# Optimization experiments

Measured on AMD Instinct MI355X. Metric: run time of the kernel, lower is better.

## Reference

```python
import jax, jax.numpy as jnp
import numpy as np

EPS = 1e-8
MARGIN = 0.2
LAMBDA_SM_LSE = 6.0   # i2t attention smooth (opt.lambda_softmax_lse)
LAMBDA_SM_AVG = 9.0   # t2i attention smooth (opt.lambda_softmax_avg)
LAMBDA_LSE = 6.0      # LogSumExp aggregation temperature
NEG = -1e9


def _l2norm(x, axis):
    return x / (jnp.sqrt(jnp.sum(x * x, axis=axis, keepdims=True)) + EPS)


def _cos(a, b):
    # cosine over last axis, torch-style: w12 / clamp(|a||b|, eps)
    w12 = jnp.sum(a * b, axis=-1)
    w1 = jnp.sqrt(jnp.sum(a * a, axis=-1))
    w2 = jnp.sqrt(jnp.sum(b * b, axis=-1))
    return w12 / jnp.maximum(w1 * w2, EPS)


def _forward(im, s, s_l):
    B, R, D = im.shape
    W = s.shape[1]
    wmask = jnp.arange(W)[None, :] < s_l[:, None]          # (Bc, W) valid words
    s = s * wmask[:, :, None]                              # emulate ragged slice s[j,:len_j]

    # ---------------- i2t: query=image regions, context=caption words ----------
    # attn[i,j,w,r] = <s[j,w], im[i,r]>
    A = jnp.einsum('jwd,ird->ijwr', s, im)
    A = jax.nn.leaky_relu(A, 0.1)
    A = _l2norm(A, axis=3)                                 # clipped_l2norm over regions
    logits = jnp.swapaxes(A, 2, 3) * LAMBDA_SM_LSE         # (i,j,r,w), softmax over words
    logits = jnp.where(wmask[None, :, None, :], logits, NEG)
    attn_i2t = jax.nn.softmax(logits, axis=-1)
    wc_t = jnp.einsum('ijrw,jwd->ijrd', attn_i2t, s)       # weighted caption ctx per region
    sim1 = _cos(im[:, None, :, :], wc_t)                   # (i,j,r)
    score1 = jnp.log(jnp.sum(jnp.exp(LAMBDA_LSE * sim1), axis=2)) / LAMBDA_LSE  # (i,j)
    attn_t_full = jnp.mean(wc_t, axis=2)                   # (i,j,d)
    idx = jnp.arange(B)
    attn_t = attn_t_full[idx, idx]                         # (B,d) diagonal

    # ---------------- t2i: query=caption words, context=image regions ----------
    # attn[i,j,r,w] = <im[i,r], s[j,w]>
    Bm = jnp.einsum('ird,jwd->ijrw', im, s)
    Bm = jax.nn.leaky_relu(Bm, 0.1)
    Bm = Bm * wmask[None, :, None, :]                      # padded-word cols excluded from norm
    Bm = _l2norm(Bm, axis=3)                               # clipped_l2norm over words
    logits2 = jnp.swapaxes(Bm, 2, 3) * LAMBDA_SM_AVG       # (i,j,w,r), softmax over regions
    attn_t2i = jax.nn.softmax(logits2, axis=-1)
    wc_i = jnp.einsum('ijwr,ird->ijwd', attn_t2i, im)      # weighted image ctx per word
    sim2 = _cos(s[None, :, :, :], wc_i)                    # (i,j,w)
    e2 = jnp.where(wmask[None, :, :], jnp.exp(LAMBDA_LSE * sim2), 0.0)
    score2 = jnp.log(jnp.sum(e2, axis=2)) / LAMBDA_LSE     # masked LogSumExp over words
    wsum = jnp.sum(wc_i * wmask[None, :, :, None], axis=2)
    attn_i_full = wsum / s_l[None, :, None].astype(wc_i.dtype)  # masked mean over words
    attn_i = attn_i_full[idx, idx]                         # (B,d)

    # ---------------- hinge loss over (B,B) score matrix -----------------------
    scores = 0.5 * (score1 + score2)
    diag = jnp.diagonal(scores)
    cost_s = jnp.maximum(MARGIN + scores - diag[:, None], 0.0)
    cost_im = jnp.maximum(MARGIN + scores - diag[None, :], 0.0)
    eye = jnp.eye(B, dtype=bool)
    cost_s = jnp.where(eye, 0.0, cost_s)
    cost_im = jnp.where(eye, 0.0, cost_im)
    # max_violation=True
    loss = jnp.sum(jnp.max(cost_s, axis=1)) + jnp.sum(jnp.max(cost_im, axis=0))
    return loss, attn_t, attn_i


def setup_inputs() -> dict:
    key = jax.random.key(0)
    k1, k2, k3 = jax.random.split(key, 3)
    B, R, W, D = 64, 36, 40, 1024
    im = jax.random.normal(k1, (B, R, D), dtype=jnp.float32)
    s = jax.random.normal(k2, (B, W, D), dtype=jnp.float32)
    s_l = jax.random.randint(k3, (B,), 10, W + 1)
    return {"im": im, "s": s, "s_l": s_l}


def reference(im, s, s_l):
    return _forward(im, s, s_l)
```

## Files before the change

### kernel.cpp

```cpp
#include <hip/hip_runtime.h>
#include <math.h>

#define Bn 64
#define Rr 36
#define Ww 40
#define Dd 1024
#define GM 2304
#define GN 2560
#define NCONV 4864
#define PAD 72
#define SBP 64
#define TSZ 1440
#define EPSf 1e-8f

typedef unsigned short u16;
typedef __attribute__((ext_vector_type(8))) short bf16x8;
typedef __attribute__((ext_vector_type(4))) float f32x4;

struct alignas(8) U16x4 { u16 x, y, z, w; };

__device__ inline u16 f2bf(float x) {
    unsigned int u = __float_as_uint(x);
    u += 0x7FFFu + ((u >> 16) & 1u);
    return (u16)(u >> 16);
}
__device__ inline float bf2f(u16 h) {
    return __uint_as_float(((unsigned int)h) << 16);
}

__device__ __forceinline__ void gl_lds16(const u16* g, u16* l) {
    __builtin_amdgcn_global_load_lds(
        (const __attribute__((address_space(1))) void*)g,
        (__attribute__((address_space(3))) void*)l, 16, 0, 0);
}

__global__ __launch_bounds__(256) void prep_kernel(const float* __restrict__ im,
                                                   const float* __restrict__ s,
                                                   const int* __restrict__ s_l,
                                                   u16* __restrict__ Ab,
                                                   u16* __restrict__ Bb,
                                                   u16* __restrict__ SSb,
                                                   u16* __restrict__ IIb,
                                                   float* __restrict__ SSd,
                                                   float* __restrict__ IId) {
    __shared__ float red[3][64][37];
    int b = blockIdx.x, t = threadIdx.x;
    if (b < NCONV) {
        const int nA4 = GM * Dd / 4;
        int idx = b * 256 + t;
        if (idx < nA4) {
            float4 v = *(const float4*)(im + (size_t)idx * 4);
            U16x4 o = {f2bf(v.x), f2bf(v.y), f2bf(v.z), f2bf(v.w)};
            *(U16x4*)(Ab + (size_t)idx * 4) = o;
        } else {
            int i2 = idx - nA4;
            int f = i2 * 4;
            int row = f >> 10;
            int j = row / Ww, w = row - j * Ww;
            U16x4 o = {0, 0, 0, 0};
            if (w < s_l[j]) {
                float4 v = *(const float4*)(s + (size_t)f);
                o.x = f2bf(v.x); o.y = f2bf(v.y); o.z = f2bf(v.z); o.w = f2bf(v.w);
            }
            *(U16x4*)(Bb + (size_t)i2 * 4) = o;
        }
        return;
    }
    int gb = b - NCONV;
    bool isS = gb < Bn;
    int idx = isS ? gb : gb - Bn;
    int n = isS ? Ww : Rr;
    const float* basef = isS ? (s + (size_t)idx * Ww * Dd) : (im + (size_t)idx * Rr * Dd);
    u16* outb = isS ? (SSb + (size_t)idx * 48 * SBP) : (IIb + (size_t)idx * 48 * SBP);
    float* outd = isS ? (SSd + (size_t)idx * Ww) : (IId + (size_t)idx * Rr);
    int lane = t & 63, wid = t >> 6;
    int frow = lane & 15, fk = (lane >> 4) * 8;

    f32x4 acc[3][3];
    for (int m = 0; m < 3; ++m)
        for (int p = 0; p < 3; ++p) acc[m][p] = (f32x4){0.f, 0.f, 0.f, 0.f};

    for (int ks = 0; ks < 8; ++ks) {
        int k0 = wid * 256 + ks * 32 + fk;
        bf16x8 f[3];
        for (int m = 0; m < 3; ++m) {
            int rr = m * 16 + frow;
            if (rr >= n) rr = n - 1;
            const float* p = basef + (size_t)rr * Dd + k0;
            float4 v0 = *(const float4*)p;
            float4 v1 = *(const float4*)(p + 4);
            bf16x8 fv;
            fv[0] = (short)f2bf(v0.x); fv[1] = (short)f2bf(v0.y);
            fv[2] = (short)f2bf(v0.z); fv[3] = (short)f2bf(v0.w);
            fv[4] = (short)f2bf(v1.x); fv[5] = (short)f2bf(v1.y);
            fv[6] = (short)f2bf(v1.z); fv[7] = (short)f2bf(v1.w);
            f[m] = fv;
        }
        for (int m = 0; m < 3; ++m)
            for (int p = 0; p < 3; ++p)
                acc[m][p] = __builtin_amdgcn_mfma_f32_16x16x32_bf16(f[m], f[p], acc[m][p], 0, 0, 0);
    }
    if (wid) {
        for (int m = 0; m < 3; ++m)
            for (int p = 0; p < 3; ++p)
                for (int q = 0; q < 4; ++q)
                    red[wid - 1][lane][(m * 3 + p) * 4 + q] = acc[m][p][q];
    }
    __syncthreads();
    if (wid == 0) {
        for (int wv = 0; wv < 3; ++wv)
            for (int m = 0; m < 3; ++m)
                for (int p = 0; p < 3; ++p)
                    for (int q = 0; q < 4; ++q)
                        acc[m][p][q] += red[wv][lane][(m * 3 + p) * 4 + q];
        int crow = (lane >> 4) * 4, ccol = lane & 15;
        for (int m = 0; m < 3; ++m)
            for (int p = 0; p < 3; ++p)
                for (int q = 0; q < 4; ++q) {
                    int row = m * 16 + crow + q;
                    int col = p * 16 + ccol;
                    float v = acc[m][p][q];
                    outb[row * SBP + col] = f2bf(v);
                    if (row == col && row < n) outd[row] = v;
                }
    }
}

__global__ __launch_bounds__(256) void gemm_mfma_kernel(const u16* __restrict__ Ab,
                                                        const u16* __restrict__ Bb,
                                                        u16* __restrict__ Gt) {
    __shared__ __align__(16) u16 As[2][64][64];
    __shared__ __align__(16) u16 Bs[2][128][64];
    int bn = blockIdx.x;
    int bm = blockIdx.y;
    int t = threadIdx.x;
    int lane = t & 63, wid = t >> 6;
    int wr = wid >> 1, wc = wid & 1;

    int lrow8 = lane >> 3;
    int sslot = (lane & 7) ^ lrow8;
    const u16* ga = Ab + ((size_t)(bm * 64 + wid * 16) + lrow8) * Dd + sslot * 8;
    const u16* gb = Bb + ((size_t)(bn * 128 + wid * 32) + lrow8) * Dd + sslot * 8;

    f32x4 acc[2][4];
    for (int m = 0; m < 2; ++m)
        for (int n = 0; n < 4; ++n) acc[m][n] = (f32x4){0.f, 0.f, 0.f, 0.f};

    int frow = lane & 15;
    int cgr = lane >> 4;

#define STAGE(BI, KK) do { \
        gl_lds16(ga + (KK), &As[BI][wid * 16][0]); \
        gl_lds16(ga + (size_t)8 * Dd + (KK), &As[BI][wid * 16 + 8][0]); \
        gl_lds16(gb + (KK), &Bs[BI][wid * 32][0]); \
        gl_lds16(gb + (size_t)8 * Dd + (KK), &Bs[BI][wid * 32 + 8][0]); \
        gl_lds16(gb + (size_t)16 * Dd + (KK), &Bs[BI][wid * 32 + 16][0]); \
        gl_lds16(gb + (size_t)24 * Dd + (KK), &Bs[BI][wid * 32 + 24][0]); \
    } while (0)

    STAGE(0, 0);
    for (int step = 0; step < 16; ++step) {
        int cur = step & 1;
        __syncthreads();
        if (step < 15) STAGE(cur ^ 1, (step + 1) * 64);
        bf16x8 af[2][2], bf[4][2];
#pragma unroll
        for (int m = 0; m < 2; ++m) {
            int row = wr * 32 + m * 16 + frow;
#pragma unroll
            for (int ks = 0; ks < 2; ++ks) {
                int slot = (ks * 4 + cgr) ^ (row & 7);
                af[m][ks] = *(const bf16x8*)&As[cur][row][slot * 8];
            }
        }
#pragma unroll
        for (int n = 0; n < 4; ++n) {
            int row = wc * 64 + n * 16 + frow;
#pragma unroll
            for (int ks = 0; ks < 2; ++ks) {
                int slot = (ks * 4 + cgr) ^ (row & 7);
                bf[n][ks] = *(const bf16x8*)&Bs[cur][row][slot * 8];
            }
        }
#pragma unroll
        for (int ks = 0; ks < 2; ++ks)
#pragma unroll
            for (int m = 0; m < 2; ++m)
#pragma unroll
                for (int n = 0; n < 4; ++n)
                    acc[m][n] = __builtin_amdgcn_mfma_f32_16x16x32_bf16(af[m][ks], bf[n][ks], acc[m][n], 0, 0, 0);
    }
#undef STAGE

    int crow0 = bm * 64 + wr * 32 + (lane >> 4) * 4;
    int ccol0 = bn * 128 + wc * 64 + (lane & 15);
    int tjv[4], wv[4];
#pragma unroll
    for (int n = 0; n < 4; ++n) {
        int col = ccol0 + n * 16;
        tjv[n] = col / 40;
        wv[n] = col - tjv[n] * 40;
    }
    for (int m = 0; m < 2; ++m)
        for (int q = 0; q < 4; ++q) {
            int row = crow0 + m * 16 + q;
            int ti = row / 36, r2 = row - ti * 36;
            u16* dstbase = Gt + (size_t)ti * Bn * TSZ + (size_t)r2 * 40;
            for (int n = 0; n < 4; ++n)
                dstbase[(size_t)tjv[n] * TSZ + wv[n]] = f2bf(acc[m][n][q]);
        }
}

__device__ __forceinline__ void quad_mfma(const u16* att, const u16* M,
                                          float* qout, int nq, int lane) {
    int c = lane & 15, g4 = lane >> 4;
    f32x4 acc[3][3];
#pragma unroll
    for (int m = 0; m < 3; ++m)
#pragma unroll
        for (int p = 0; p < 3; ++p) acc[m][p] = (f32x4){0.f, 0.f, 0.f, 0.f};
#pragma unroll
    for (int ks = 0; ks < 2; ++ks) {
        bf16x8 fa[3], fb[3];
#pragma unroll
        for (int m = 0; m < 3; ++m)
            fa[m] = *(const bf16x8*)&att[(m * 16 + c) * PAD + g4 * 8 + ks * 32];
#pragma unroll
        for (int p = 0; p < 3; ++p)
            fb[p] = *(const bf16x8*)(M + (size_t)(p * 16 + c) * SBP + g4 * 8 + ks * 32);
#pragma unroll
        for (int m = 0; m < 3; ++m)
#pragma unroll
            for (int p = 0; p < 3; ++p)
                acc[m][p] = __builtin_amdgcn_mfma_f32_16x16x32_bf16(fa[m], fb[p], acc[m][p], 0, 0, 0);
    }
#pragma unroll
    for (int m = 0; m < 3; ++m)
#pragma unroll
        for (int q = 0; q < 4; ++q) {
            int row = m * 16 + g4 * 4 + q;
            float sp = 0.f;
#pragma unroll
            for (int p = 0; p < 3; ++p)
                sp += acc[m][p][q] * bf2f(att[row * PAD + p * 16 + c]);
            sp += __shfl_xor(sp, 1);
            sp += __shfl_xor(sp, 2);
            sp += __shfl_xor(sp, 4);
            sp += __shfl_xor(sp, 8);
            if (c == 0 && row < nq) qout[row] = sp;
        }
}

__global__ __launch_bounds__(128) void pair_kernel(const u16* __restrict__ Gt,
                                                   const u16* __restrict__ SSb,
                                                   const u16* __restrict__ IIb,
                                                   const float* __restrict__ SSd,
                                                   const float* __restrict__ IId,
                                                   const int* __restrict__ s_l,
                                                   float* __restrict__ score1,
                                                   float* __restrict__ score2,
                                                   float* __restrict__ dAp,
                                                   float* __restrict__ dBp) {
    int j = blockIdx.x, i = blockIdx.y;
    int t = threadIdx.x, lane = t & 63, wid = t >> 6;
    __shared__ __align__(16) u16 glb[Rr * 44];
    __shared__ __align__(16) u16 attA[48 * PAD];
    __shared__ __align__(16) u16 attB[48 * PAD];
    __shared__ float invA[Ww], invB[Rr], sA[Rr], sB[Ww], qA[Rr], qB[Ww];
    int L = s_l[j];

    {
        uint* za = (uint*)attA;
        uint* zb = (uint*)attB;
#pragma unroll
        for (int k = 0; k < 14; ++k) {
            int idx = t + k * 128;
            if (idx < 48 * PAD / 2) { za[idx] = 0; zb[idx] = 0; }
        }
        const u16* gt = Gt + (size_t)(i * Bn + j) * TSZ;
        for (int c = t; c < 180; c += 128) {
            int r = c / 5, q = c - (c / 5) * 5;
            uint4 v = *(const uint4*)(gt + c * 8);
            *(uint2*)&glb[r * 44 + q * 8] = make_uint2(v.x, v.y);
            *(uint2*)&glb[r * 44 + q * 8 + 4] = make_uint2(v.z, v.w);
        }
    }
    float iid = 0.f, ssd = 0.f;
    if (wid == 0 && lane < Rr) iid = IId[i * Rr + lane];
    if (wid == 1 && lane < Ww) ssd = SSd[j * Ww + lane];
    __syncthreads();

    if (wid == 0 && lane < Rr) {
        float sum = 0.f;
#pragma unroll 8
        for (int w = 0; w < Ww; ++w) {
            float x = bf2f(glb[lane * 44 + w]);
            x = x < 0.f ? 0.1f * x : x;
            sum += x * x;
        }
        invB[lane] = 9.f / (sqrtf(sum) + EPSf);
    }
    if (wid == 1 && lane < Ww) {
        float sum = 0.f;
#pragma unroll 6
        for (int r = 0; r < Rr; ++r) {
            float x = bf2f(glb[r * 44 + lane]);
            x = x < 0.f ? 0.1f * x : x;
            sum += x * x;
        }
        invA[lane] = 6.f / (sqrtf(sum) + EPSf);
    }
    __syncthreads();

    float dot = 0.f, myinv = 0.f;
    if (wid == 0 && lane < Rr) {
        float ssum = 0.f;
#pragma unroll 8
        for (int w = 0; w < Ww; ++w) {
            float e = 0.f;
            if (w < L) {
                float gx = bf2f(glb[lane * 44 + w]);
                float x = gx < 0.f ? 0.1f * gx : gx;
                e = __expf(x * invA[w]);
                dot += e * gx;
            }
            attA[lane * PAD + w] = f2bf(e);
            ssum += e;
        }
        myinv = 1.f / ssum;
        dot *= myinv;
        sA[lane] = myinv;
    }
    if (wid == 1 && lane < Ww) {
        float ssum = 0.f;
#pragma unroll 6
        for (int r = 0; r < Rr; ++r) {
            float gx = bf2f(glb[r * 44 + lane]);
            float x = gx < 0.f ? 0.1f * gx : gx;
            float e = __expf(x * invB[r]);
            dot += e * gx;
            attB[lane * PAD + r] = f2bf(e);
            ssum += e;
        }
        myinv = 1.f / ssum;
        dot *= myinv;
        sB[lane] = myinv;
    }
    __syncthreads();

    if (wid == 0)
        quad_mfma(attA, SSb + (size_t)j * 48 * SBP, qA, Rr, lane);
    else
        quad_mfma(attB, IIb + (size_t)i * 48 * SBP, qB, Ww, lane);

    if (wid == 0) {
        float e1 = 0.f;
        if (lane < Rr) {
            float q = qA[lane] * myinv * myinv;
            float s1 = dot / fmaxf(sqrtf(iid) * sqrtf(fmaxf(q, 0.f)), EPSf);
            e1 = __expf(6.f * s1);
        }
#pragma unroll
        for (int off = 1; off < 64; off <<= 1) e1 += __shfl_xor(e1, off);
        if (lane == 0) score1[i * Bn + j] = __logf(e1) * (1.f / 6.f);
    } else {
        float e2 = 0.f;
        if (lane < Ww) {
            float q = qB[lane] * myinv * myinv;
            float s2 = dot / fmaxf(sqrtf(ssd) * sqrtf(fmaxf(q, 0.f)), EPSf);
            e2 = (lane < L) ? __expf(6.f * s2) : 0.f;
        }
#pragma unroll
        for (int off = 1; off < 64; off <<= 1) e2 += __shfl_xor(e2, off);
        if (lane == 0) score2[i * Bn + j] = __logf(e2) * (1.f / 6.f);
    }

    if (i == j) {
        __syncthreads();
        if (wid == 1 && lane < Ww) {
            float sum = 0.f;
#pragma unroll 6
            for (int r = 0; r < Rr; ++r) sum += bf2f(attA[r * PAD + lane]) * sA[r];
            dAp[i * Ww + lane] = sum * (1.f / (float)Rr);
        }
        if (wid == 0 && lane < Rr) {
            float sum = 0.f;
            for (int w = 0; w < L; ++w) sum += bf2f(attB[w * PAD + lane]) * sB[w];
            dBp[i * Rr + lane] = sum / (float)L;
        }
    }
}

__global__ __launch_bounds__(256) void diag_out_kernel(const u16* __restrict__ Ab,
                                                       const u16* __restrict__ Bb,
                                                       const int* __restrict__ s_l,
                                                       const float* __restrict__ dA,
                                                       const float* __restrict__ dB,
                                                       const float* __restrict__ score1,
                                                       const float* __restrict__ score2,
                                                       float* __restrict__ out) {
    int t = threadIdx.x;
    if (blockIdx.y == 4) {
        if (blockIdx.x != 0) return;
        __shared__ float sc[Bn][Bn + 1];
        for (int idx = t; idx < Bn * Bn; idx += 256)
            sc[idx >> 6][idx & 63] = 0.5f * (score1[idx] + score2[idx]);
        __syncthreads();
        if (t < 64) {
            float dt = sc[t][t];
            float rowmax = 0.f, colmax = 0.f;
            for (int k = 0; k < Bn; ++k) {
                if (k != t) {
                    rowmax = fmaxf(rowmax, 0.2f + sc[t][k] - dt);
                    colmax = fmaxf(colmax, 0.2f + sc[k][t] - dt);
                }
            }
            float v = rowmax + colmax;
            for (int off = 32; off; off >>= 1) v += __shfl_down(v, off);
            if (t == 0) out[0] = v;
        }
        return;
    }
    int i = blockIdx.x;
    int d = blockIdx.y * 256 + t;
    int L = s_l[i];
    __shared__ float aw[Ww], br[Rr];
    if (t < Ww) aw[t] = dA[i * Ww + t];
    if (t >= 64 && t < 64 + Rr) br[t - 64] = dB[i * Rr + (t - 64)];
    __syncthreads();
    float acc1 = 0.f;
    for (int w = 0; w < L; ++w) acc1 += aw[w] * bf2f(Bb[((size_t)i * Ww + w) * Dd + d]);
    out[1 + (size_t)i * Dd + d] = acc1;
    float acc2 = 0.f;
    for (int r = 0; r < Rr; ++r) acc2 += br[r] * bf2f(Ab[((size_t)i * Rr + r) * Dd + d]);
    out[1 + (size_t)Bn * Dd + (size_t)i * Dd + d] = acc2;
}

extern "C" void kernel_launch(void* const* d_in, const int* in_sizes, int n_in,
                              void* d_out, int out_size, void* d_ws, size_t ws_size,
                              hipStream_t stream) {
    const float* im = (const float*)d_in[0];
    const float* s = (const float*)d_in[1];
    const int* s_l = (const int*)d_in[2];
    float* out = (float*)d_out;

    u16* Ab = (u16*)d_ws;
    u16* Bb = Ab + (size_t)GM * Dd;
    u16* Gt = Bb + (size_t)GN * Dd;
    u16* SSb = Gt + (size_t)GM * GN;
    u16* IIb = SSb + (size_t)Bn * 48 * SBP;
    float* SSd = (float*)(IIb + (size_t)Bn * 48 * SBP);
    float* IId = SSd + (size_t)Bn * Ww;
    float* score1 = IId + (size_t)Bn * Rr;
    float* score2 = score1 + Bn * Bn;
    float* dA = score2 + Bn * Bn;
    float* dB = dA + Bn * Ww;

    prep_kernel<<<NCONV + 2 * Bn, 256, 0, stream>>>(im, s, s_l, Ab, Bb, SSb, IIb, SSd, IId);

    dim3 ggrid(GN / 128, GM / 64);
    gemm_mfma_kernel<<<ggrid, 256, 0, stream>>>(Ab, Bb, Gt);

    dim3 pgrid(Bn, Bn);
    pair_kernel<<<pgrid, 128, 0, stream>>>(Gt, SSb, IIb, SSd, IId, s_l,
                                           score1, score2, dA, dB);

    dim3 dgrid(Bn, 5);
    diag_out_kernel<<<dgrid, 256, 0, stream>>>(Ab, Bb, s_l, dA, dB, score1, score2, out);
}
```

Measured before the change: 77.14 us.

## Triple-buffer GEMM LDS pipeline and vectorize diagonal output kernel

Result: slower. 78.94 us (+2.3%).

```diff
diff --git a/kernel.cpp b/kernel.cpp
--- a/kernel.cpp
+++ b/kernel.cpp
@@ -129,8 +129,8 @@
 __global__ __launch_bounds__(256) void gemm_mfma_kernel(const u16* __restrict__ Ab,
                                                         const u16* __restrict__ Bb,
                                                         u16* __restrict__ Gt) {
-    __shared__ __align__(16) u16 As[2][64][64];
-    __shared__ __align__(16) u16 Bs[2][128][64];
+    __shared__ __align__(16) u16 As[3][64][64];
+    __shared__ __align__(16) u16 Bs[3][128][64];
     int bn = blockIdx.x;
     int bm = blockIdx.y;
     int t = threadIdx.x;
@@ -159,10 +159,15 @@
     } while (0)
 
     STAGE(0, 0);
-    for (int step = 0; step < 16; ++step) {
-        int cur = step & 1;
-        __syncthreads();
-        if (step < 15) STAGE(cur ^ 1, (step + 1) * 64);
+    STAGE(1, 64);
+#pragma unroll
+    for (int s = 0; s < 16; ++s) {
+        if (s < 15) asm volatile("s_waitcnt vmcnt(6)" ::: "memory");
+        else        asm volatile("s_waitcnt vmcnt(0)" ::: "memory");
+        __builtin_amdgcn_sched_barrier(0);
+        __builtin_amdgcn_s_barrier();
+        __builtin_amdgcn_sched_barrier(0);
+        const int cur = s % 3;
         bf16x8 af[2][2], bf[4][2];
 #pragma unroll
         for (int m = 0; m < 2; ++m) {
@@ -182,6 +187,7 @@
                 bf[n][ks] = *(const bf16x8*)&Bs[cur][row][slot * 8];
             }
         }
+        if (s + 2 < 16) STAGE((s + 2) % 3, (s + 2) * 64);
 #pragma unroll
         for (int ks = 0; ks < 2; ++ks)
 #pragma unroll
@@ -189,6 +195,8 @@
 #pragma unroll
                 for (int n = 0; n < 4; ++n)
                     acc[m][n] = __builtin_amdgcn_mfma_f32_16x16x32_bf16(af[m][ks], bf[n][ks], acc[m][n], 0, 0, 0);
+        asm volatile("s_waitcnt lgkmcnt(0)" ::: "memory");
+        __builtin_amdgcn_sched_barrier(0);
     }
 #undef STAGE
 
@@ -391,7 +399,7 @@
     }
 }
 
-__global__ __launch_bounds__(256) void diag_out_kernel(const u16* __restrict__ Ab,
+__global__ __launch_bounds__(128) void diag_out_kernel(const u16* __restrict__ Ab,
                                                        const u16* __restrict__ Bb,
                                                        const int* __restrict__ s_l,
                                                        const float* __restrict__ dA,
@@ -400,10 +408,10 @@
                                                        const float* __restrict__ score2,
                                                        float* __restrict__ out) {
     int t = threadIdx.x;
-    if (blockIdx.y == 4) {
-        if (blockIdx.x != 0) return;
+    int bi = blockIdx.x;
+    if (bi == Bn) {
         __shared__ float sc[Bn][Bn + 1];
-        for (int idx = t; idx < Bn * Bn; idx += 256)
+        for (int idx = t; idx < Bn * Bn; idx += 128)
             sc[idx >> 6][idx & 63] = 0.5f * (score1[idx] + score2[idx]);
         __syncthreads();
         if (t < 64) {
@@ -421,19 +429,35 @@
         }
         return;
     }
-    int i = blockIdx.x;
-    int d = blockIdx.y * 256 + t;
+    int i = bi;
     int L = s_l[i];
     __shared__ float aw[Ww], br[Rr];
     if (t < Ww) aw[t] = dA[i * Ww + t];
     if (t >= 64 && t < 64 + Rr) br[t - 64] = dB[i * Rr + (t - 64)];
     __syncthreads();
-    float acc1 = 0.f;
-    for (int w = 0; w < L; ++w) acc1 += aw[w] * bf2f(Bb[((size_t)i * Ww + w) * Dd + d]);
-    out[1 + (size_t)i * Dd + d] = acc1;
-    float acc2 = 0.f;
-    for (int r = 0; r < Rr; ++r) acc2 += br[r] * bf2f(Ab[((size_t)i * Rr + r) * Dd + d]);
-    out[1 + (size_t)Bn * Dd + (size_t)i * Dd + d] = acc2;
+    int d0 = t * 8;
+    const u16* BbI = Bb + (size_t)i * Ww * Dd + d0;
+    const u16* AbI = Ab + (size_t)i * Rr * Dd + d0;
+    float a1[8], a2[8];
+#pragma unroll
+    for (int k = 0; k < 8; ++k) { a1[k] = 0.f; a2[k] = 0.f; }
+    for (int w = 0; w < L; ++w) {
+        bf16x8 v = *(const bf16x8*)(BbI + (size_t)w * Dd);
+        float c = aw[w];
+#pragma unroll
+        for (int k = 0; k < 8; ++k) a1[k] += c * bf2f((u16)v[k]);
+    }
+#pragma unroll 6
+    for (int r = 0; r < Rr; ++r) {
+        bf16x8 v = *(const bf16x8*)(AbI + (size_t)r * Dd);
+        float c = br[r];
+#pragma unroll
+        for (int k = 0; k < 8; ++k) a2[k] += c * bf2f((u16)v[k]);
+    }
+    float* o1 = out + 1 + (size_t)i * Dd + d0;
+    float* o2 = out + 1 + (size_t)Bn * Dd + (size_t)i * Dd + d0;
+#pragma unroll
+    for (int k = 0; k < 8; ++k) { o1[k] = a1[k]; o2[k] = a2[k]; }
 }
 
 extern "C" void kernel_launch(void* const* d_in, const int* in_sizes, int n_in,
@@ -465,6 +489,5 @@
     pair_kernel<<<pgrid, 128, 0, stream>>>(Gt, SSb, IIb, SSd, IId, s_l,
                                            score1, score2, dA, dB);
 
-    dim3 dgrid(Bn, 5);
-    diag_out_kernel<<<dgrid, 256, 0, stream>>>(Ab, Bb, s_l, dA, dB, score1, score2, out);
-}
+    diag_out_kernel<<<Bn + 1, 128, 0, stream>>>(Ab, Bb, s_l, dA, dB, score1, score2, out);
+}
```
